# Performance work log

Measured on AMD Instinct MI355X. Metric: run time of the kernel, lower is better.

The kernel has to match this reference:

```python
import jax, jax.numpy as jnp
import numpy as np
from jax import lax

H = 128  # LSTM hidden size (hardcoded in module)

def setup_inputs() -> dict:
    key = jax.random.key(0)
    ks = jax.random.split(key, 10)
    B, S, D = 256, 512, 80
    T = 3
    s_in = 1.0 / np.sqrt(D)
    s_h = 1.0 / np.sqrt(H)
    return {
        "x": jax.random.normal(ks[0], (B, S, D), dtype=jnp.float32),
        "W_in": jax.random.uniform(ks[1], (256, D), jnp.float32, -s_in, s_in),
        "b_in": jax.random.uniform(ks[2], (256,), jnp.float32, -s_in, s_in),
        "W_ih": jax.random.uniform(ks[3], (4 * H, 256), jnp.float32, -s_h, s_h),
        "b_ih": jax.random.uniform(ks[4], (4 * H,), jnp.float32, -s_h, s_h),
        "W_hh": jax.random.uniform(ks[5], (4 * H, H), jnp.float32, -s_h, s_h),
        "b_hh": jax.random.uniform(ks[6], (4 * H,), jnp.float32, -s_h, s_h),
        "w_time": jax.random.uniform(ks[7], (T,), jnp.float32, -1.0 / np.sqrt(T), 1.0 / np.sqrt(T)),
        "W_br": jax.random.uniform(ks[8], (4, H), jnp.float32, -s_h, s_h),
        "b_br": jax.random.uniform(ks[9], (4,), jnp.float32, -s_h, s_h),
        "batch_size": B,
        "time_steps": T,
    }


def reference(x, W_in, b_in, W_ih, b_ih, W_hh, b_hh, w_time, W_br, b_br, batch_size, time_steps):
    # input projection (dropout is identity in eval mode)
    xl = jnp.einsum('bsd,ed->bse', x, W_in) + b_in  # [B,S,256]
    B, S, _ = xl.shape
    T = time_steps

    def step(carry, inp):
        h, c, h_st, c_st = carry
        xt, i = inp  # xt: [B,256], i: step index
        gates = xt @ W_ih.T + b_ih + h @ W_hh.T + b_hh  # [B,4H]
        ig, fg, gg, og = jnp.split(gates, 4, axis=-1)
        c_new = jax.nn.sigmoid(fg) * c + jax.nn.sigmoid(ig) * jnp.tanh(gg)
        h_new = jax.nn.sigmoid(og) * jnp.tanh(c_new)
        slot = i % T
        oh = jax.nn.one_hot(slot, T, dtype=h_new.dtype)  # [T]
        h_st = h_st * (1.0 - oh) + h_new[:, :, None] * oh  # [B,H,T]
        c_st = c_st * (1.0 - oh) + c_new[:, :, None] * oh
        pool = (slot == T - 1)
        ph = jnp.einsum('bht,t->bh', h_st, w_time)
        pc = jnp.einsum('bht,t->bh', c_st, w_time)
        h_out = jnp.where(pool, ph, h_new)
        c_out = jnp.where(pool, pc, c_new)
        h_st = jnp.where(pool, jnp.zeros_like(h_st), h_st)
        c_st = jnp.where(pool, jnp.zeros_like(c_st), c_st)
        return (h_out, c_out, h_st, c_st), h_out

    init = (jnp.zeros((B, H), xl.dtype), jnp.zeros((B, H), xl.dtype),
            jnp.zeros((B, H, T), xl.dtype), jnp.zeros((B, H, T), xl.dtype))
    _, outs = lax.scan(step, init, (jnp.swapaxes(xl, 0, 1), jnp.arange(S)))
    out = jnp.swapaxes(outs, 0, 1)  # [B,S,H]
    logits = jnp.einsum('bsh,oh->bso', out, W_br) + b_br  # [B,S,4]
    return jax.nn.log_softmax(logits, axis=2)
```

## Files before the change

### kernel.cpp

```cpp
#include <hip/hip_runtime.h>
#include <hip/hip_fp16.h>

#define BB 256
#define SS 512
#define DD 80
#define HH 128
#define GG 512

typedef _Float16 h2_t __attribute__((ext_vector_type(2)));

union U32H2 { unsigned int u; h2_t h; unsigned short us[2]; };

static __device__ __forceinline__ h2_t u2h(unsigned int u) { U32H2 x; x.u = u; return x.h; }

static __device__ __forceinline__ unsigned int pk2(float a, float b) {
  unsigned int lo = (unsigned int)__half_as_ushort(__float2half(a));
  unsigned int hi = (unsigned int)__half_as_ushort(__float2half(b));
  return (hi << 16) | lo;
}

static __device__ __forceinline__ float fdot2(unsigned int a, unsigned int b, float c) {
#if __has_builtin(__builtin_amdgcn_fdot2)
  return __builtin_amdgcn_fdot2(u2h(a), u2h(b), c, false);
#else
  U32H2 ua, ub; ua.u = a; ub.u = b;
  return c + (float)ua.h[0] * (float)ub.h[0] + (float)ua.h[1] * (float)ub.h[1];
#endif
}

static __device__ __forceinline__ float fsig(float x) {
  return __fdividef(1.f, 1.f + __expf(-x));
}
static __device__ __forceinline__ float ftanh(float x) {
  x = fminf(fmaxf(x, -15.f), 15.f);
  float e = __expf(2.f * x);
  return __fdividef(e - 1.f, e + 1.f);
}

__global__ __launch_bounds__(128) void prep_kernel(
    const float* __restrict__ W_in, const float* __restrict__ b_in,
    const float* __restrict__ W_ih, const float* __restrict__ b_ih,
    const float* __restrict__ W_hh, const float* __restrict__ b_hh,
    unsigned short* __restrict__ wc16, unsigned short* __restrict__ whh16,
    float* __restrict__ biasc)
{
  const int g = blockIdx.x;
  const int t = threadIdx.x;
  const float* wih = W_ih + g * 256;
  if (t < DD) {
    float s = 0.f;
    for (int e = 0; e < 256; ++e) s += wih[e] * W_in[e * DD + t];
    wc16[g * DD + t] = __half_as_ushort(__float2half(s));
  }
  whh16[g * HH + t] = __half_as_ushort(__float2half(W_hh[g * HH + t]));
  if (t == 0) {
    float s = 0.f;
    for (int e = 0; e < 256; ++e) s += wih[e] * b_in[e];
    biasc[g] = s + b_ih[g] + b_hh[g];
  }
}

__global__ __launch_bounds__(256) void gemm_kernel(
    const float* __restrict__ x,
    const unsigned short* __restrict__ wc16,
    uint4* __restrict__ gx)
{
  __shared__ unsigned int Al[40][64];
  __shared__ unsigned int Bl[40][256];
  const int t  = threadIdx.x;
  const int mt = blockIdx.x;
  const int g0 = blockIdx.y * 256;

  {
    const int mm = t & 63, kq = t >> 6;
    const float* xr = x + ((size_t)mt * 64 + mm) * DD + kq * 20;
    #pragma unroll
    for (int p = 0; p < 10; ++p)
      Al[kq * 10 + p][mm] = pk2(xr[2 * p], xr[2 * p + 1]);
  }
  {
    const unsigned int* wr = (const unsigned int*)wc16 + (size_t)(g0 + t) * 40;
    #pragma unroll
    for (int k = 0; k < 40; ++k) Bl[k][t] = wr[k];
  }
  __syncthreads();

  const int mb = (t >> 5) * 8;
  const int gb = (t & 31) * 4;
  float acc[8][8];
  #pragma unroll
  for (int i = 0; i < 8; ++i)
    #pragma unroll
    for (int j = 0; j < 8; ++j) acc[i][j] = 0.f;

  #pragma unroll 5
  for (int kk = 0; kk < 40; ++kk) {
    uint4 a0 = *(const uint4*)&Al[kk][mb];
    uint4 a1 = *(const uint4*)&Al[kk][mb + 4];
    uint4 b0 = *(const uint4*)&Bl[kk][gb];
    uint4 b1 = *(const uint4*)&Bl[kk][gb + 128];
    unsigned int aa[8] = {a0.x, a0.y, a0.z, a0.w, a1.x, a1.y, a1.z, a1.w};
    unsigned int bb[8] = {b0.x, b0.y, b0.z, b0.w, b1.x, b1.y, b1.z, b1.w};
    #pragma unroll
    for (int i = 0; i < 8; ++i)
      #pragma unroll
      for (int j = 0; j < 8; ++j)
        acc[i][j] = fdot2(aa[i], bb[j], acc[i][j]);
  }

  const size_t rb = (size_t)mt * 8 + (t >> 5);
  #pragma unroll
  for (int jj = 0; jj < 2; ++jj) {
    #pragma unroll
    for (int j = 0; j < 4; ++j) {
      const int jc = jj * 4 + j;
      uint4 o;
      o.x = pk2(acc[0][jc], acc[1][jc]);
      o.y = pk2(acc[2][jc], acc[3][jc]);
      o.z = pk2(acc[4][jc], acc[5][jc]);
      o.w = pk2(acc[6][jc], acc[7][jc]);
      gx[rb * 512 + (size_t)(g0 + jj * 128 + gb + j)] = o;
    }
  }
}

__global__ __launch_bounds__(512) void scan_kernel(
    const uint4* __restrict__ gx,
    const uint4* __restrict__ whh,
    const float* __restrict__ biasc,
    const float* __restrict__ wtime,
    __half* __restrict__ hout)
{
  __shared__ unsigned int hpk[64];
  __shared__ float act[512];
  const int b = blockIdx.x;
  const int t = threadIdx.x;

  unsigned int w[64];
  {
    const uint4* wr = whh + (size_t)t * 16;
    #pragma unroll
    for (int i = 0; i < 16; ++i) {
      uint4 v = wr[i];
      w[4*i] = v.x; w[4*i+1] = v.y; w[4*i+2] = v.z; w[4*i+3] = v.w;
    }
  }
  const float bias = biasc[t];
  const float wt0 = wtime[0], wt1 = wtime[1], wt2 = wtime[2];
  if (t < 64) hpk[t] = 0u;
  float c = 0.f, hst0 = 0.f, hst1 = 0.f, cst0 = 0.f, cst1 = 0.f;
  int slot = 0;
  int s = 0;
  const uint4* gxp = gx + (size_t)b * 64 * 512 + t;
  __syncthreads();

  uint4 gxv = gxp[0];
  for (int sb = 0; sb < 64; ++sb) {
    uint4 gxn;
    if (sb < 63) gxn = gxp[(size_t)(sb + 1) * 512];
    unsigned int ga[4] = {gxv.x, gxv.y, gxv.z, gxv.w};
    #pragma unroll
    for (int i = 0; i < 8; ++i) {
      const unsigned int hreg = hpk[t & 63];
      U32H2 gu; gu.u = ga[i >> 1];
      const float gxi = (float)gu.h[i & 1];
      float ac0 = bias + gxi, ac1 = 0.f, ac2 = 0.f, ac3 = 0.f;
      #pragma unroll
      for (int p = 0; p < 64; p += 4) {
        unsigned int h0 = (unsigned int)__builtin_amdgcn_readlane((int)hreg, p);
        unsigned int h1 = (unsigned int)__builtin_amdgcn_readlane((int)hreg, p + 1);
        unsigned int h2 = (unsigned int)__builtin_amdgcn_readlane((int)hreg, p + 2);
        unsigned int h3 = (unsigned int)__builtin_amdgcn_readlane((int)hreg, p + 3);
        ac0 = fdot2(w[p],     h0, ac0);
        ac1 = fdot2(w[p + 1], h1, ac1);
        ac2 = fdot2(w[p + 2], h2, ac2);
        ac3 = fdot2(w[p + 3], h3, ac3);
      }
      const float accv = (ac0 + ac1) + (ac2 + ac3);
      const float a = (t >= 256 && t < 384) ? ftanh(accv) : fsig(accv);
      act[t] = a;
      __syncthreads();
      if (t < 128) {
        const float ig = act[t], fg = act[t + 128], gg = act[t + 256], og = act[t + 384];
        c = fg * c + ig * gg;
        const float hn = og * ftanh(c);
        float hcur;
        if (slot == 2) {
          hcur = hst0 * wt0 + hst1 * wt1 + hn * wt2;
          c    = cst0 * wt0 + cst1 * wt1 + c  * wt2;
        } else {
          hcur = hn;
          if (slot == 0) { hst0 = hn; cst0 = c; }
          else           { hst1 = hn; cst1 = c; }
        }
        const __half hh = __float2half(hcur);
        ((__half*)hpk)[t] = hh;
        hout[((size_t)b * SS + s) * HH + t] = hh;
      }
      slot = (slot == 2) ? 0 : slot + 1;
      ++s;
      __syncthreads();
    }
    gxv = gxn;
  }
}

__global__ __launch_bounds__(256) void out_kernel(
    const uint4* __restrict__ hout,
    const float* __restrict__ Wbr, const float* __restrict__ bbr,
    float4* __restrict__ out)
{
  __shared__ unsigned int wb[4][64];
  __shared__ float bbs[4];
  const int t = threadIdx.x;
  {
    const int o = t >> 6, p = t & 63;
    wb[o][p] = pk2(Wbr[o * HH + 2 * p], Wbr[o * HH + 2 * p + 1]);
  }
  if (t < 4) bbs[t] = bbr[t];
  __syncthreads();

  const size_t row = (size_t)blockIdx.x * 256 + t;
  const uint4* hr = hout + row * 16;
  float a0 = bbs[0], a1 = bbs[1], a2 = bbs[2], a3 = bbs[3];
  #pragma unroll
  for (int q = 0; q < 16; ++q) {
    uint4 hv = hr[q];
    unsigned int hd[4] = {hv.x, hv.y, hv.z, hv.w};
    #pragma unroll
    for (int d = 0; d < 4; ++d) {
      const int p = q * 4 + d;
      a0 = fdot2(hd[d], wb[0][p], a0);
      a1 = fdot2(hd[d], wb[1][p], a1);
      a2 = fdot2(hd[d], wb[2][p], a2);
      a3 = fdot2(hd[d], wb[3][p], a3);
    }
  }
  const float m = fmaxf(fmaxf(a0, a1), fmaxf(a2, a3));
  const float e0 = __expf(a0 - m), e1 = __expf(a1 - m), e2 = __expf(a2 - m), e3 = __expf(a3 - m);
  const float lse = m + __logf(e0 + e1 + e2 + e3);
  out[row] = make_float4(a0 - lse, a1 - lse, a2 - lse, a3 - lse);
}

extern "C" void kernel_launch(void* const* d_in, const int* in_sizes, int n_in,
                              void* d_out, int out_size, void* d_ws, size_t ws_size,
                              hipStream_t stream) {
  const float* x     = (const float*)d_in[0];
  const float* W_in  = (const float*)d_in[1];
  const float* b_in  = (const float*)d_in[2];
  const float* W_ih  = (const float*)d_in[3];
  const float* b_ih  = (const float*)d_in[4];
  const float* W_hh  = (const float*)d_in[5];
  const float* b_hh  = (const float*)d_in[6];
  const float* wtime = (const float*)d_in[7];
  const float* W_br  = (const float*)d_in[8];
  const float* b_br  = (const float*)d_in[9];
  (void)in_sizes; (void)n_in; (void)out_size; (void)ws_size;

  char* ws = (char*)d_ws;
  unsigned short* wc16  = (unsigned short*)(ws + 0);
  unsigned short* whh16 = (unsigned short*)(ws + 81920);
  float*          biasc = (float*)(ws + 212992);
  __half*         hout  = (__half*)(ws + 215040);
  uint4*          gx    = (uint4*)(ws + 33769472);

  prep_kernel<<<512, 128, 0, stream>>>(W_in, b_in, W_ih, b_ih, W_hh, b_hh,
                                       wc16, whh16, biasc);
  gemm_kernel<<<dim3(2048, 2), 256, 0, stream>>>(x, wc16, gx);
  scan_kernel<<<256, 512, 0, stream>>>(gx, (const uint4*)whh16, biasc, wtime, hout);
  out_kernel<<<512, 256, 0, stream>>>((const uint4*)hout, W_br, b_br, (float4*)d_out);
}
```

Baseline: 646.1 us.

## Split LSTM gates across thread pairs to drop one barrier per step

The scan kernel now runs 256 threads per batch row, with each thread computing two gate rows (64+64 registers of W_hh). Gate activations are exchanged between adjacent lanes with a shuffle instead of going through shared memory, so one of the two block barriers per timestep goes away. Hidden state is double-buffered in LDS, and tanh is rewritten as 2*sigmoid(2x)-1. The trade-off is double the register pressure and dot-product work per thread, with half as many waves available to hide latency.

```diff
diff --git a/kernel.cpp b/kernel.cpp
--- a/kernel.cpp
+++ b/kernel.cpp
@@ -30,11 +30,6 @@
 
 static __device__ __forceinline__ float fsig(float x) {
   return __fdividef(1.f, 1.f + __expf(-x));
-}
-static __device__ __forceinline__ float ftanh(float x) {
-  x = fminf(fmaxf(x, -15.f), 15.f);
-  float e = __expf(2.f * x);
-  return __fdividef(e - 1.f, e + 1.f);
 }
 
 __global__ __launch_bounds__(128) void prep_kernel(
@@ -124,84 +119,109 @@
   }
 }
 
-__global__ __launch_bounds__(512) void scan_kernel(
+__global__ __launch_bounds__(256, 1) void scan_kernel(
     const uint4* __restrict__ gx,
     const uint4* __restrict__ whh,
     const float* __restrict__ biasc,
     const float* __restrict__ wtime,
     __half* __restrict__ hout)
 {
-  __shared__ unsigned int hpk[64];
-  __shared__ float act[512];
-  const int b = blockIdx.x;
-  const int t = threadIdx.x;
-
-  unsigned int w[64];
-  {
-    const uint4* wr = whh + (size_t)t * 16;
+  __shared__ unsigned int hbuf[2][64];
+  const int b    = blockIdx.x;
+  const int t    = threadIdx.x;
+  const int lane = t & 63;
+  const int hi   = t >> 1;
+  const int odd  = t & 1;
+  const int g1   = odd * 128 + hi;
+  const int g2   = g1 + 256;
+
+  unsigned int w1[64], w2[64];
+  {
+    const uint4* wr1 = whh + (size_t)g1 * 16;
+    const uint4* wr2 = whh + (size_t)g2 * 16;
     #pragma unroll
     for (int i = 0; i < 16; ++i) {
-      uint4 v = wr[i];
-      w[4*i] = v.x; w[4*i+1] = v.y; w[4*i+2] = v.z; w[4*i+3] = v.w;
-    }
-  }
-  const float bias = biasc[t];
+      uint4 v = wr1[i];
+      w1[4*i] = v.x; w1[4*i+1] = v.y; w1[4*i+2] = v.z; w1[4*i+3] = v.w;
+      uint4 u = wr2[i];
+      w2[4*i] = u.x; w2[4*i+1] = u.y; w2[4*i+2] = u.z; w2[4*i+3] = u.w;
+    }
+  }
+  const float bias1 = biasc[g1];
+  const float bias2 = biasc[g2];
   const float wt0 = wtime[0], wt1 = wtime[1], wt2 = wtime[2];
-  if (t < 64) hpk[t] = 0u;
+  if (t < 64) { hbuf[0][t] = 0u; hbuf[1][t] = 0u; }
   float c = 0.f, hst0 = 0.f, hst1 = 0.f, cst0 = 0.f, cst1 = 0.f;
-  int slot = 0;
-  int s = 0;
-  const uint4* gxp = gx + (size_t)b * 64 * 512 + t;
+  int slot = 0, s = 0;
+  const uint4* gxp1 = gx + (size_t)b * 64 * 512 + g1;
+  const uint4* gxp2 = gx + (size_t)b * 64 * 512 + g2;
   __syncthreads();
 
-  uint4 gxv = gxp[0];
+  uint4 gv1 = gxp1[0];
+  uint4 gv2 = gxp2[0];
   for (int sb = 0; sb < 64; ++sb) {
-    uint4 gxn;
-    if (sb < 63) gxn = gxp[(size_t)(sb + 1) * 512];
-    unsigned int ga[4] = {gxv.x, gxv.y, gxv.z, gxv.w};
+    uint4 gn1, gn2;
+    if (sb < 63) {
+      gn1 = gxp1[(size_t)(sb + 1) * 512];
+      gn2 = gxp2[(size_t)(sb + 1) * 512];
+    }
+    unsigned int ga1[4] = {gv1.x, gv1.y, gv1.z, gv1.w};
+    unsigned int ga2[4] = {gv2.x, gv2.y, gv2.z, gv2.w};
     #pragma unroll
     for (int i = 0; i < 8; ++i) {
-      const unsigned int hreg = hpk[t & 63];
-      U32H2 gu; gu.u = ga[i >> 1];
-      const float gxi = (float)gu.h[i & 1];
-      float ac0 = bias + gxi, ac1 = 0.f, ac2 = 0.f, ac3 = 0.f;
+      const int par = s & 1;
+      const unsigned int hreg = hbuf[par][lane];
+      U32H2 u1; u1.u = ga1[i >> 1];
+      U32H2 u2; u2.u = ga2[i >> 1];
+      const float gxi1 = (float)u1.h[i & 1];
+      const float gxi2 = (float)u2.h[i & 1];
+      float d1a = bias1 + gxi1, d1b = 0.f;
+      float d2a = bias2 + gxi2, d2b = 0.f;
       #pragma unroll
-      for (int p = 0; p < 64; p += 4) {
+      for (int p = 0; p < 64; p += 2) {
         unsigned int h0 = (unsigned int)__builtin_amdgcn_readlane((int)hreg, p);
         unsigned int h1 = (unsigned int)__builtin_amdgcn_readlane((int)hreg, p + 1);
-        unsigned int h2 = (unsigned int)__builtin_amdgcn_readlane((int)hreg, p + 2);
-        unsigned int h3 = (unsigned int)__builtin_amdgcn_readlane((int)hreg, p + 3);
-        ac0 = fdot2(w[p],     h0, ac0);
-        ac1 = fdot2(w[p + 1], h1, ac1);
-        ac2 = fdot2(w[p + 2], h2, ac2);
-        ac3 = fdot2(w[p + 3], h3, ac3);
+        d1a = fdot2(w1[p],     h0, d1a);
+        d2a = fdot2(w2[p],     h0, d2a);
+        d1b = fdot2(w1[p + 1], h1, d1b);
+        d2b = fdot2(w2[p + 1], h1, d2b);
       }
-      const float accv = (ac0 + ac1) + (ac2 + ac3);
-      const float a = (t >= 256 && t < 384) ? ftanh(accv) : fsig(accv);
-      act[t] = a;
-      __syncthreads();
-      if (t < 128) {
-        const float ig = act[t], fg = act[t + 128], gg = act[t + 256], og = act[t + 384];
-        c = fg * c + ig * gg;
-        const float hn = og * ftanh(c);
-        float hcur;
-        if (slot == 2) {
-          hcur = hst0 * wt0 + hst1 * wt1 + hn * wt2;
-          c    = cst0 * wt0 + cst1 * wt1 + c  * wt2;
-        } else {
-          hcur = hn;
-          if (slot == 0) { hst0 = hn; cst0 = c; }
-          else           { hst1 = hn; cst1 = c; }
-        }
+      const float d1 = d1a + d1b;
+      const float d2 = d2a + d2b;
+      const float a1 = fsig(d1);
+      const float yin = odd ? d2 : (d2 + d2);
+      const float sv  = fsig(yin);
+      const float a2  = odd ? sv : (2.f * sv - 1.f);
+      const float p1 = __shfl_xor(a1, 1);
+      const float p2 = __shfl_xor(a2, 1);
+      const float iv = odd ? p1 : a1;
+      const float gg = odd ? p2 : a2;
+      const float fv = odd ? a1 : p1;
+      const float ov = odd ? a2 : p2;
+      c = fv * c + iv * gg;
+      const float tc = 2.f * fsig(c + c) - 1.f;
+      const float hn = ov * tc;
+      float hcur;
+      if (slot == 2) {
+        hcur = hst0 * wt0 + hst1 * wt1 + hn * wt2;
+        c    = cst0 * wt0 + cst1 * wt1 + c  * wt2;
+        slot = 0;
+      } else {
+        hcur = hn;
+        if (slot == 0) { hst0 = hn; cst0 = c; }
+        else           { hst1 = hn; cst1 = c; }
+        ++slot;
+      }
+      if (!odd) {
         const __half hh = __float2half(hcur);
-        ((__half*)hpk)[t] = hh;
-        hout[((size_t)b * SS + s) * HH + t] = hh;
+        ((__half*)hbuf[par ^ 1])[hi] = hh;
+        hout[((size_t)b * SS + s) * HH + hi] = hh;
       }
-      slot = (slot == 2) ? 0 : slot + 1;
       ++s;
       __syncthreads();
     }
-    gxv = gxn;
+    gv1 = gn1;
+    gv2 = gn2;
   }
 }
 
@@ -267,6 +287,6 @@
   prep_kernel<<<512, 128, 0, stream>>>(W_in, b_in, W_ih, b_ih, W_hh, b_hh,
                                        wc16, whh16, biasc);
   gemm_kernel<<<dim3(2048, 2), 256, 0, stream>>>(x, wc16, gx);
-  scan_kernel<<<256, 512, 0, stream>>>(gx, (const uint4*)whh16, biasc, wtime, hout);
+  scan_kernel<<<256, 256, 0, stream>>>(gx, (const uint4*)whh16, biasc, wtime, hout);
   out_kernel<<<512, 256, 0, stream>>>((const uint4*)hout, W_br, b_br, (float4*)d_out);
 }
```

Result: faster. 609.3 us (-5.7%).
